# Performance work log

Hardware: AMD Instinct MI355X
Metric: run time of the kernel (lower is better)

Reference implementation:

```python
import jax, jax.numpy as jnp
import numpy as np

IN_FEATURES = 512
OUT_FEATURES = 256
BATCH = 1024


def setup_inputs() -> dict:
    key = jax.random.key(0)
    k1, k2, k3, k4 = jax.random.split(key, 4)
    n_lower = IN_FEATURES * (IN_FEATURES - 1) // 2  # strictly-lower triangle count
    return {
        "inputs": jax.random.normal(k1, (BATCH, IN_FEATURES), dtype=jnp.float32),
        "weight": jax.random.normal(k2, (OUT_FEATURES, 1, IN_FEATURES), dtype=jnp.float32),
        "L_diags": jax.random.uniform(k3, (OUT_FEATURES, IN_FEATURES), dtype=jnp.float32),
        "L_lower": jax.random.normal(k4, (OUT_FEATURES, n_lower), dtype=jnp.float32) * 0.05,
    }


def _build_L(L_diags, L_lower):
    # Per-class lower-triangular matrix: diag = L_diags**2, strict lower = L_lower.
    K, d = L_diags.shape
    ri, ci = np.tril_indices(d, k=-1)  # static index pattern (row-major, matches torch.tril_indices)
    diag_idx = jnp.arange(d)
    L = jnp.zeros((K, d, d), dtype=L_diags.dtype)
    L = L.at[:, diag_idx, diag_idx].set(jnp.square(L_diags))
    L = L.at[:, ri, ci].set(L_lower)
    return L  # [K, d, d]


def reference(inputs, weight, L_diags, L_lower):
    L = _build_L(L_diags, L_lower)                      # [K, d, d]
    pinputs = jnp.einsum('bd,kde->kbe', inputs, L)      # [K, B, d]
    pweights = jnp.einsum('kod,kde->koe', weight, L)    # [K, 1, d]
    dist = pinputs - pweights                           # broadcast over B -> [K, B, d]
    out = jnp.sqrt(jnp.sum(jnp.square(dist), axis=2))   # torch.norm(dim=2) -> [K, B]
    return out.T                                        # [B, K]
```

## Files before the change

kernel.cpp:

```cpp
#include <hip/hip_runtime.h>
#include <hip/hip_bf16.h>
#include <math.h>

#define B_SZ   1024
#define D_SZ   512
#define KC_SZ  256
#define NLOW   130816

#define STEP_ELEMS  8192
#define NSTEPS      20
#define CLASS_ELEMS (NSTEPS * STEP_ELEMS)

#define OFF_XP     (size_t)(KC_SZ * CLASS_ELEMS * 2)
#define OFF_TPART  (OFF_XP + 64 * STEP_ELEMS * 2)
#define OFF_T      (OFF_TPART + (size_t)KC_SZ * 8 * 512 * 4)
#define WS_NEED    (OFF_T + (size_t)KC_SZ * 512 * 4)

typedef __attribute__((ext_vector_type(4))) float  f32x4;
typedef __attribute__((ext_vector_type(4), aligned(4))) float f32x4u;
typedef __attribute__((ext_vector_type(8))) __bf16 bf16x8;

__device__ __forceinline__ int sbase_of(int ct) { return ct * (9 - ct); }
__device__ __forceinline__ int kch_of(int s) {
    return (s < 8) ? s : (s < 14) ? s - 6 : (s < 18) ? s - 10 : s - 12;
}

__global__ __launch_bounds__(256)
void prep_x(const float* __restrict__ X, __hip_bfloat16* __restrict__ Xp) {
    const int bx  = blockIdx.x;
    const int pg  = bx >> 2;
    const int mt  = pg >> 3, kch = pg & 7;
    __bf16* out = (__bf16*)Xp + (size_t)pg * STEP_ELEMS;
    const int line = threadIdx.x + (bx & 3) * 256;
    const int wmg = line >> 9, mi = (line >> 7) & 3, h = (line >> 6) & 1;
    const int lane = line & 63, q = lane >> 4, c = lane & 15;
    const int row = mt * 128 + wmg * 64 + mi * 16 + c;
    const float* src = X + (size_t)row * D_SZ + kch * 64 + h * 32 + q * 8;
    f32x4 v0 = ((const f32x4*)src)[0];
    f32x4 v1 = ((const f32x4*)src)[1];
    bf16x8 p;
    #pragma unroll
    for (int j = 0; j < 4; ++j) { p[j] = (__bf16)v0[j]; p[j + 4] = (__bf16)v1[j]; }
    *(bf16x8*)(out + line * 8) = p;
}

__global__ __launch_bounds__(256)
void prep_b(const float* __restrict__ Ldiag,
            const float* __restrict__ Llow,
            const float* __restrict__ W,
            __hip_bfloat16* __restrict__ Bp,
            float* __restrict__ tpart) {
    __shared__ __bf16 Lt[128 * 64];
    __shared__ float  ptl[32 * 129];

    const int s  = blockIdx.x;
    const int kc = blockIdx.y;
    const int ct = (s < 8) ? 0 : (s < 14) ? 1 : (s < 18) ? 2 : 3;
    const int dt = kch_of(s);
    const int e0 = ct << 7, d0 = dt << 6;

    const int tid = threadIdx.x;
    const int m   = tid & 31;
    const int seg = tid >> 5;
    const int es  = seg << 4;
    const int dg0 = d0 + 2 * m;

    int cls;
    if (dt >= 2 * ct + 2)      cls = 0;
    else if (dt == 2 * ct + 1) cls = (seg < 4) ? 0 : 1;
    else                       cls = (seg < 4) ? 1 : 2;

    const float* lowb = Llow + (size_t)kc * NLOW;
    const float2 wv = *(const float2*)(W + (size_t)kc * D_SZ + dg0);

    float v0[16], v1[16];
    if (cls == 0) {
        const int t0 = (dg0 * (dg0 - 1)) >> 1;
        const int t1 = t0 + dg0;
        const float* s0 = lowb + t0 + e0 + es;
        const float* s1 = lowb + t1 + e0 + es;
        #pragma unroll
        for (int i = 0; i < 4; ++i) {
            f32x4u a = ((const f32x4u*)s0)[i];
            f32x4u b = ((const f32x4u*)s1)[i];
            #pragma unroll
            for (int j = 0; j < 4; ++j) { v0[i * 4 + j] = a[j]; v1[i * 4 + j] = b[j]; }
        }
    } else if (cls == 1) {
        const int t0 = (dg0 * (dg0 - 1)) >> 1;
        const int t1 = t0 + dg0;
        const float* diagb = Ldiag + (size_t)kc * D_SZ;
        float q0 = diagb[dg0],     q1 = diagb[dg0 + 1];
        q0 *= q0; q1 *= q1;
        #pragma unroll
        for (int j = 0; j < 16; ++j) {
            const int eg = e0 + es + j;
            v0[j] = (eg < dg0)     ? lowb[t0 + eg] : ((eg == dg0)     ? q0 : 0.f);
            v1[j] = (eg < dg0 + 1) ? lowb[t1 + eg] : ((eg == dg0 + 1) ? q1 : 0.f);
        }
    } else {
        #pragma unroll
        for (int j = 0; j < 16; ++j) { v0[j] = 0.f; v1[j] = 0.f; }
    }

    char* ltb = (char*)Lt;
    #pragma unroll
    for (int j = 0; j < 16; ++j) {
        const int el = es + j;
        union { __bf16 h[2]; unsigned u; } pk;
        pk.h[0] = (__bf16)v0[j];
        pk.h[1] = (__bf16)v1[j];
        const int off = el * 128 + ((4 * m) ^ ((el & 7) << 4));
        *(unsigned*)(ltb + off) = pk.u;
        ptl[m * 129 + el] = wv.x * v0[j] + wv.y * v1[j];
    }
    __syncthreads();

    __bf16* page = (__bf16*)Bp + (size_t)kc * CLASS_ELEMS + (size_t)s * STEP_ELEMS;
    const int lane = tid & 63, q = lane >> 4, c = lane & 15;
    #pragma unroll
    for (int k = 0; k < 4; ++k) {
        const int ln = k * 256 + tid;
        const int up = ln >> 6;
        const int h  = up & 1;
        const int el = ((up >> 3) << 6) + (((up >> 1) & 3) << 4) + c;
        const int off = el * 128 + (((h << 6) + (q << 4)) ^ ((el & 7) << 4));
        *(bf16x8*)(page + (size_t)ln * 8) = *(const bf16x8*)(ltb + off);
    }

    if (tid < 128) {
        float sum = 0.f;
        #pragma unroll
        for (int mm = 0; mm < 32; ++mm) sum += ptl[mm * 129 + tid];
        tpart[((size_t)(kc * 8 + dt)) * 512 + e0 + tid] = sum;
    }
}

__global__ __launch_bounds__(256)
void t_reduce(const float* __restrict__ tpart, float* __restrict__ Tv) {
    const int idx = blockIdx.x * 256 + threadIdx.x;
    const int kc = idx >> 9, e = idx & 511;
    const int ct = e >> 7;
    float s = 0.f;
    for (int dt = ct << 1; dt < 8; ++dt)
        s += tpart[((size_t)(kc * 8 + dt)) * 512 + e];
    Tv[idx] = s;
}

__global__ __launch_bounds__(256, 2)
void gml2_main(const __hip_bfloat16* __restrict__ Xp,
               const __hip_bfloat16* __restrict__ Bp,
               const float* __restrict__ Tv,
               float* __restrict__ Out) {
    __shared__ __align__(16) char ldsbuf[2][32768];

    const int tid = threadIdx.x;
    const int bx  = blockIdx.x;
    const int xcd = bx & 7;
    const int g   = bx >> 3;
    const int kc  = xcd * 32 + (g >> 3);
    const int mt  = g & 7;

    const int lane = tid & 63;
    const int wave = tid >> 6;
    const int wmg  = wave & 1;
    const int wng  = wave >> 1;
    const int c    = lane & 15;
    const int q    = lane >> 4;

    const __bf16* pA = (const __bf16*)Xp + (size_t)(mt * 8) * STEP_ELEMS;
    const __bf16* pB = (const __bf16*)Bp + (size_t)kc * CLASS_ELEMS;

    float tvr[4][4];
    #pragma unroll
    for (int ct4 = 0; ct4 < 4; ++ct4)
        #pragma unroll
        for (int ni = 0; ni < 4; ++ni)
            tvr[ct4][ni] = Tv[kc * 512 + ct4 * 128 + wng * 64 + ni * 16 + c];

    int aoff[4][2], boff[4][2];
    #pragma unroll
    for (int mi = 0; mi < 4; ++mi)
        #pragma unroll
        for (int h = 0; h < 2; ++h)
            aoff[mi][h] = (((wmg * 4 + mi) * 2 + h) * 64 + lane) * 16;
    #pragma unroll
    for (int ni = 0; ni < 4; ++ni)
        #pragma unroll
        for (int h = 0; h < 2; ++h)
            boff[ni][h] = (((wng * 4 + ni) * 2 + h) * 64 + lane) * 16;

    f32x4 acc[4][4];
    #pragma unroll
    for (int mi = 0; mi < 4; ++mi)
        #pragma unroll
        for (int ni = 0; ni < 4; ++ni)
            acc[mi][ni] = (f32x4){0.f, 0.f, 0.f, 0.f};
    float rsum[16];
    #pragma unroll
    for (int i = 0; i < 16; ++i) rsum[i] = 0.f;

    bf16x8 fa[4][2], fb[4][2];

#define STAGE(BUF, SIDX) {                                                     \
    const int kch_ = kch_of(SIDX);                                             \
    const char* ga_ = (const char*)(pA + (size_t)kch_ * STEP_ELEMS);           \
    const char* gb_ = (const char*)(pB + (size_t)(SIDX) * STEP_ELEMS);         \
    char* la_ = &ldsbuf[BUF][0];                                               \
    char* lb_ = &ldsbuf[BUF][16384];                                           \
    _Pragma("unroll") for (int i_ = 0; i_ < 4; ++i_) {                         \
        const int ch_ = (wave * 4 + i_) * 1024;                                \
        __builtin_amdgcn_global_load_lds(                                      \
            (const __attribute__((address_space(1))) void*)(ga_ + ch_ + lane * 16), \
            (__attribute__((address_space(3))) void*)(la_ + ch_), 16, 0, 0);   \
        __builtin_amdgcn_global_load_lds(                                      \
            (const __attribute__((address_space(1))) void*)(gb_ + ch_ + lane * 16), \
            (__attribute__((address_space(3))) void*)(lb_ + ch_), 16, 0, 0);   \
    } }

#define LDS_FRAGS(BUF) {                                                       \
    const char* la_ = &ldsbuf[BUF][0];                                         \
    const char* lb_ = &ldsbuf[BUF][16384];                                     \
    _Pragma("unroll") for (int mi = 0; mi < 4; ++mi)                           \
    _Pragma("unroll") for (int h = 0; h < 2; ++h)                              \
        fa[mi][h] = *(const bf16x8*)(la_ + aoff[mi][h]);                       \
    _Pragma("unroll") for (int ni = 0; ni < 4; ++ni)                           \
    _Pragma("unroll") for (int h = 0; h < 2; ++h)                              \
        fb[ni][h] = *(const bf16x8*)(lb_ + boff[ni][h]); }

#define MFMA_ALL                                                               \
    _Pragma("unroll") for (int mi = 0; mi < 4; ++mi)                           \
    _Pragma("unroll") for (int ni = 0; ni < 4; ++ni)                           \
    _Pragma("unroll") for (int h = 0; h < 2; ++h)                              \
        acc[mi][ni] = __builtin_amdgcn_mfma_f32_16x16x32_bf16(                 \
            fa[mi][h], fb[ni][h], acc[mi][ni], 0, 0, 0);

#define FOLD(CT) {                                                             \
    _Pragma("unroll") for (int mi = 0; mi < 4; ++mi)                           \
    _Pragma("unroll") for (int ni = 0; ni < 4; ++ni)                           \
    _Pragma("unroll") for (int r = 0; r < 4; ++r) {                            \
        float y_ = acc[mi][ni][r] - tvr[CT][ni];                               \
        rsum[mi * 4 + r] += y_ * y_;                                           \
        acc[mi][ni][r] = 0.f; } }

    STAGE(0, 0);

    #pragma unroll
    for (int s = 0; s < NSTEPS; ++s) {
        const int cur = s & 1;
        if (s == 8)       { FOLD(0); }
        else if (s == 14) { FOLD(1); }
        else if (s == 18) { FOLD(2); }

        if (s + 1 < NSTEPS) {
            STAGE(cur ^ 1, s + 1);
            asm volatile("s_waitcnt vmcnt(8)" ::: "memory");
        } else {
            asm volatile("s_waitcnt vmcnt(0)" ::: "memory");
        }
        __builtin_amdgcn_s_barrier();

        LDS_FRAGS(cur);
        MFMA_ALL;

        __builtin_amdgcn_s_barrier();
    }
    FOLD(3);

    #pragma unroll
    for (int i = 0; i < 16; ++i) {
        float v = rsum[i];
        v += __shfl_xor(v, 1, 64);
        v += __shfl_xor(v, 2, 64);
        v += __shfl_xor(v, 4, 64);
        v += __shfl_xor(v, 8, 64);
        rsum[i] = v;
    }
    float (*osum)[128] = (float(*)[128])&ldsbuf[0][0];
    if (c == 0) {
        #pragma unroll
        for (int mi = 0; mi < 4; ++mi)
            #pragma unroll
            for (int r = 0; r < 4; ++r)
                osum[wng][wmg * 64 + mi * 16 + q * 4 + r] = rsum[mi * 4 + r];
    }
    __syncthreads();
    if (tid < 128) {
        float v = osum[0][tid] + osum[1][tid];
        Out[(size_t)(mt * 128 + tid) * KC_SZ + kc] = sqrtf(v);
    }
}

#define FLDA 40
#define BM 128
#define BN 128
__device__ __forceinline__ void fstep_map(int s, int& ct, int& k0) {
    if (s < 16)      { ct = 0; k0 = s * 32; }
    else if (s < 28) { ct = 1; k0 = 128 + (s - 16) * 32; }
    else if (s < 36) { ct = 2; k0 = 256 + (s - 28) * 32; }
    else             { ct = 3; k0 = 384 + (s - 36) * 32; }
}
__global__ __launch_bounds__(256, 2)
void gml2_fallback(const float* __restrict__ X, const float* __restrict__ W,
                   const float* __restrict__ Ldiag, const float* __restrict__ Llow,
                   float* __restrict__ Out) {
    __shared__ __bf16 As[BM * FLDA];
    __shared__ __bf16 Bs[BN * FLDA];
    __shared__ float  Ws[D_SZ];
    __shared__ float  osum[2][BM];
    const int tid = threadIdx.x;
    const int bx  = blockIdx.x;
    const int xcd = bx & 7;
    const int g   = bx >> 3;
    const int kc  = xcd * 32 + (g >> 3);
    const int mt  = g & 7;
    const int lane = tid & 63, wave = tid >> 6;
    const int wm = (wave & 1) * 64, wn = (wave >> 1) * 64;
    const int c = lane & 15, q = lane >> 4;
    const int am = tid >> 1, akh = (tid & 1) << 4;
    const float* xrow = X + (size_t)(mt * BM + am) * D_SZ;
    const float* wrow = W + (size_t)kc * D_SZ;
    const int be = tid & 127, bd = (tid >> 7) << 4;
    const float* lowbase  = Llow  + (size_t)kc * NLOW;
    const float* diagbase = Ldiag + (size_t)kc * D_SZ;
    if (tid < 128) ((f32x4*)Ws)[tid] = ((const f32x4*)wrow)[tid];
    float rsum[16];
    #pragma unroll
    for (int i = 0; i < 16; ++i) rsum[i] = 0.f;
    f32x4 acc[4][4];
    #pragma unroll
    for (int mi = 0; mi < 4; ++mi)
        #pragma unroll
        for (int ni = 0; ni < 4; ++ni) acc[mi][ni] = (f32x4){0.f, 0.f, 0.f, 0.f};
    f32x4 xr[4];
    float bb[16];
    auto prefetch = [&](int s) {
        int pct, pk0; fstep_map(s, pct, pk0);
        const int pe0 = pct * BN;
        const float* xp = xrow + pk0 + akh;
        #pragma unroll
        for (int i = 0; i < 4; ++i) xr[i] = ((const f32x4*)xp)[i];
        const int e = pe0 + be, d0 = pk0 + bd;
        int tri = (d0 * (d0 - 1)) >> 1;
        if (pk0 >= pe0 + BN) {
            #pragma unroll
            for (int j = 0; j < 16; ++j) { bb[j] = lowbase[tri + e]; tri += d0 + j; }
        } else {
            #pragma unroll
            for (int j = 0; j < 16; ++j) {
                const int d = d0 + j;
                float val = 0.f;
                if (d > e)       val = lowbase[tri + e];
                else if (d == e) { float dq = diagbase[d]; val = dq * dq; }
                bb[j] = val; tri += d;
            }
        }
    };
    prefetch(0);
    __syncthreads();
    int cur_ct = 0;
    for (int s = 0; s < 40; ++s) {
        int ct, k0; fstep_map(s, ct, k0);
        if (ct != cur_ct) {
            #pragma unroll
            for (int mi = 0; mi < 4; ++mi)
                #pragma unroll
                for (int ni = 0; ni < 4; ++ni)
                    #pragma unroll
                    for (int r = 0; r < 4; ++r) {
                        float y = acc[mi][ni][r];
                        rsum[mi * 4 + r] += y * y;
                        acc[mi][ni][r] = 0.f;
                    }
            cur_ct = ct;
        }
        bf16x8 ap0, ap1;
        {
            const f32x4* wsp = (const f32x4*)&Ws[k0 + akh];
            #pragma unroll
            for (int i = 0; i < 4; ++i) {
                f32x4 wv = wsp[i];
                #pragma unroll
                for (int l = 0; l < 4; ++l) {
                    float v = xr[i][l] - wv[l];
                    int idx = i * 4 + l;
                    if (idx < 8) ap0[idx] = (__bf16)v;
                    else         ap1[idx - 8] = (__bf16)v;
                }
            }
        }
        bf16x8 bp0, bp1;
        #pragma unroll
        for (int j = 0; j < 8; ++j) { bp0[j] = (__bf16)bb[j]; bp1[j] = (__bf16)bb[j + 8]; }
        __syncthreads();
        *(bf16x8*)&As[am * FLDA + akh]     = ap0;
        *(bf16x8*)&As[am * FLDA + akh + 8] = ap1;
        *(bf16x8*)&Bs[be * FLDA + bd]      = bp0;
        *(bf16x8*)&Bs[be * FLDA + bd + 8]  = bp1;
        if (s + 1 < 40) prefetch(s + 1);
        __syncthreads();
        bf16x8 af[4], bfr[4];
        #pragma unroll
        for (int mi = 0; mi < 4; ++mi)
            af[mi] = *(const bf16x8*)&As[(wm + mi * 16 + c) * FLDA + q * 8];
        #pragma unroll
        for (int ni = 0; ni < 4; ++ni)
            bfr[ni] = *(const bf16x8*)&Bs[(wn + ni * 16 + c) * FLDA + q * 8];
        #pragma unroll
        for (int mi = 0; mi < 4; ++mi)
            #pragma unroll
            for (int ni = 0; ni < 4; ++ni)
                acc[mi][ni] = __builtin_amdgcn_mfma_f32_16x16x32_bf16(
                    af[mi], bfr[ni], acc[mi][ni], 0, 0, 0);
    }
    #pragma unroll
    for (int mi = 0; mi < 4; ++mi)
        #pragma unroll
        for (int ni = 0; ni < 4; ++ni)
            #pragma unroll
            for (int r = 0; r < 4; ++r) {
                float y = acc[mi][ni][r];
                rsum[mi * 4 + r] += y * y;
            }
    #pragma unroll
    for (int i = 0; i < 16; ++i) {
        float s = rsum[i];
        s += __shfl_xor(s, 1, 64);
        s += __shfl_xor(s, 2, 64);
        s += __shfl_xor(s, 4, 64);
        s += __shfl_xor(s, 8, 64);
        rsum[i] = s;
    }
    const int wnIdx = wave >> 1;
    if (c == 0) {
        #pragma unroll
        for (int mi = 0; mi < 4; ++mi)
            #pragma unroll
            for (int r = 0; r < 4; ++r)
                osum[wnIdx][wm + mi * 16 + q * 4 + r] = rsum[mi * 4 + r];
    }
    __syncthreads();
    if (tid < BM) {
        float s = osum[0][tid] + osum[1][tid];
        Out[(size_t)(mt * BM + tid) * KC_SZ + kc] = sqrtf(s);
    }
}

extern "C" void kernel_launch(void* const* d_in, const int* in_sizes, int n_in,
                              void* d_out, int out_size, void* d_ws, size_t ws_size,
                              hipStream_t stream) {
    const float* X  = (const float*)d_in[0];
    const float* W  = (const float*)d_in[1];
    const float* Ld = (const float*)d_in[2];
    const float* Ll = (const float*)d_in[3];
    float* Out = (float*)d_out;

    if (ws_size >= WS_NEED) {
        __hip_bfloat16* Bp    = (__hip_bfloat16*)d_ws;
        __hip_bfloat16* Xp    = (__hip_bfloat16*)((char*)d_ws + OFF_XP);
        float*          tpart = (float*)((char*)d_ws + OFF_TPART);
        float*          Tvv   = (float*)((char*)d_ws + OFF_T);
        prep_x  <<<dim3(256),           dim3(256), 0, stream>>>(X, Xp);
        prep_b  <<<dim3(NSTEPS, KC_SZ), dim3(256), 0, stream>>>(Ld, Ll, W, Bp, tpart);
        t_reduce<<<dim3(512),           dim3(256), 0, stream>>>(tpart, Tvv);
        gml2_main<<<dim3(KC_SZ * 8),    dim3(256), 0, stream>>>(Xp, Bp, Tvv, Out);
    } else {
        gml2_fallback<<<dim3(KC_SZ * 8), dim3(256), 0, stream>>>(X, W, Ld, Ll, Out);
    }
}
```

Measured before the change: 302.7 us.

## Keep A-operand fragments resident in registers, stage only B through LDS

Loads all eight K-chunks of the input tile's MFMA fragments directly from global memory into registers once, before the main loop. Only the per-class B operand is now double-buffered through LDS. This halves per-step LDS staging and fragment reads, and shrinks shared memory to the B buffers plus a separate reduction array. In exchange, 256 extra VGPRs of fragment state are held per thread, which risks spilling or reduced occupancy under the two-blocks-per-CU launch bound.

```diff
diff --git a/kernel.cpp b/kernel.cpp
--- a/kernel.cpp
+++ b/kernel.cpp
@@ -152,7 +152,8 @@
                const __hip_bfloat16* __restrict__ Bp,
                const float* __restrict__ Tv,
                float* __restrict__ Out) {
-    __shared__ __align__(16) char ldsbuf[2][32768];
+    __shared__ __align__(16) char bbuf[2][16384];
+    __shared__ float osum[2][128];
 
     const int tid = threadIdx.x;
     const int bx  = blockIdx.x;
@@ -178,17 +179,15 @@
         for (int ni = 0; ni < 4; ++ni)
             tvr[ct4][ni] = Tv[kc * 512 + ct4 * 128 + wng * 64 + ni * 16 + c];
 
-    int aoff[4][2], boff[4][2];
-    #pragma unroll
-    for (int mi = 0; mi < 4; ++mi)
-        #pragma unroll
-        for (int h = 0; h < 2; ++h)
-            aoff[mi][h] = (((wmg * 4 + mi) * 2 + h) * 64 + lane) * 16;
-    #pragma unroll
-    for (int ni = 0; ni < 4; ++ni)
-        #pragma unroll
-        for (int h = 0; h < 2; ++h)
-            boff[ni][h] = (((wng * 4 + ni) * 2 + h) * 64 + lane) * 16;
+    bf16x8 fa[8][4][2];
+    #pragma unroll
+    for (int kch = 0; kch < 8; ++kch)
+        #pragma unroll
+        for (int mi = 0; mi < 4; ++mi)
+            #pragma unroll
+            for (int h = 0; h < 2; ++h)
+                fa[kch][mi][h] = *(const bf16x8*)(pA + (size_t)kch * STEP_ELEMS
+                                  + ((((wmg * 4 + mi) * 2 + h) * 64) + lane) * 8);
 
     f32x4 acc[4][4];
     #pragma unroll
@@ -200,40 +199,15 @@
     #pragma unroll
     for (int i = 0; i < 16; ++i) rsum[i] = 0.f;
 
-    bf16x8 fa[4][2], fb[4][2];
-
-#define STAGE(BUF, SIDX) {                                                     \
-    const int kch_ = kch_of(SIDX);                                             \
-    const char* ga_ = (const char*)(pA + (size_t)kch_ * STEP_ELEMS);           \
-    const char* gb_ = (const char*)(pB + (size_t)(SIDX) * STEP_ELEMS);         \
-    char* la_ = &ldsbuf[BUF][0];                                               \
-    char* lb_ = &ldsbuf[BUF][16384];                                           \
+#define STAGE_B(BUF, SP) {                                                     \
+    const char* gb_ = (const char*)(pB + (size_t)(SP) * STEP_ELEMS);           \
+    char* lb_ = &bbuf[BUF][0];                                                 \
     _Pragma("unroll") for (int i_ = 0; i_ < 4; ++i_) {                         \
         const int ch_ = (wave * 4 + i_) * 1024;                                \
-        __builtin_amdgcn_global_load_lds(                                      \
-            (const __attribute__((address_space(1))) void*)(ga_ + ch_ + lane * 16), \
-            (__attribute__((address_space(3))) void*)(la_ + ch_), 16, 0, 0);   \
         __builtin_amdgcn_global_load_lds(                                      \
             (const __attribute__((address_space(1))) void*)(gb_ + ch_ + lane * 16), \
             (__attribute__((address_space(3))) void*)(lb_ + ch_), 16, 0, 0);   \
     } }
-
-#define LDS_FRAGS(BUF) {                                                       \
-    const char* la_ = &ldsbuf[BUF][0];                                         \
-    const char* lb_ = &ldsbuf[BUF][16384];                                     \
-    _Pragma("unroll") for (int mi = 0; mi < 4; ++mi)                           \
-    _Pragma("unroll") for (int h = 0; h < 2; ++h)                              \
-        fa[mi][h] = *(const bf16x8*)(la_ + aoff[mi][h]);                       \
-    _Pragma("unroll") for (int ni = 0; ni < 4; ++ni)                           \
-    _Pragma("unroll") for (int h = 0; h < 2; ++h)                              \
-        fb[ni][h] = *(const bf16x8*)(lb_ + boff[ni][h]); }
-
-#define MFMA_ALL                                                               \
-    _Pragma("unroll") for (int mi = 0; mi < 4; ++mi)                           \
-    _Pragma("unroll") for (int ni = 0; ni < 4; ++ni)                           \
-    _Pragma("unroll") for (int h = 0; h < 2; ++h)                              \
-        acc[mi][ni] = __builtin_amdgcn_mfma_f32_16x16x32_bf16(                 \
-            fa[mi][h], fb[ni][h], acc[mi][ni], 0, 0, 0);
 
 #define FOLD(CT) {                                                             \
     _Pragma("unroll") for (int mi = 0; mi < 4; ++mi)                           \
@@ -243,25 +217,40 @@
         rsum[mi * 4 + r] += y_ * y_;                                           \
         acc[mi][ni][r] = 0.f; } }
 
-    STAGE(0, 0);
+    STAGE_B(0, 0);
 
     #pragma unroll
     for (int s = 0; s < NSTEPS; ++s) {
         const int cur = s & 1;
+        const int kch = kch_of(s);
         if (s == 8)       { FOLD(0); }
         else if (s == 14) { FOLD(1); }
         else if (s == 18) { FOLD(2); }
 
         if (s + 1 < NSTEPS) {
-            STAGE(cur ^ 1, s + 1);
-            asm volatile("s_waitcnt vmcnt(8)" ::: "memory");
+            STAGE_B(cur ^ 1, s + 1);
+            asm volatile("s_waitcnt vmcnt(4)" ::: "memory");
         } else {
             asm volatile("s_waitcnt vmcnt(0)" ::: "memory");
         }
         __builtin_amdgcn_s_barrier();
 
-        LDS_FRAGS(cur);
-        MFMA_ALL;
+        bf16x8 fb[4][2];
+        #pragma unroll
+        for (int ni = 0; ni < 4; ++ni)
+            #pragma unroll
+            for (int h = 0; h < 2; ++h)
+                fb[ni][h] = *(const bf16x8*)(&bbuf[cur][0]
+                              + ((((wng * 4 + ni) * 2 + h) * 64) + lane) * 16);
+
+        #pragma unroll
+        for (int h = 0; h < 2; ++h)
+            #pragma unroll
+            for (int mi = 0; mi < 4; ++mi)
+                #pragma unroll
+                for (int ni = 0; ni < 4; ++ni)
+                    acc[mi][ni] = __builtin_amdgcn_mfma_f32_16x16x32_bf16(
+                        fa[kch][mi][h], fb[ni][h], acc[mi][ni], 0, 0, 0);
 
         __builtin_amdgcn_s_barrier();
     }
@@ -276,7 +265,6 @@
         v += __shfl_xor(v, 8, 64);
         rsum[i] = v;
     }
-    float (*osum)[128] = (float(*)[128])&ldsbuf[0][0];
     if (c == 0) {
         #pragma unroll
         for (int mi = 0; mi < 4; ++mi)
```

Result: slower. 602.9 us (+99.2%).

## Merge prep kernels, fold T reduction into main, skip zero upper-triangle pages

Applied to the files above, without the earlier changes.

Merges prep_x and prep_b into one launch and removes the t_reduce kernel. The main kernel now reduces the T partial sums into shared memory itself. On diagonal tiles where half of the B page is zero (upper triangle), the change stages only half of B and lets only one wave-column group do the MFMAs. The goal is to cut launch overhead and redundant loads and matrix work on the triangular diagonal blocks. In exchange it adds per-block reduction work and load imbalance across waves, and it relies on the per-step vmcnt counts being correct.

```diff
diff --git a/kernel.cpp b/kernel.cpp
--- a/kernel.cpp
+++ b/kernel.cpp
@@ -26,40 +26,48 @@
 }
 
 __global__ __launch_bounds__(256)
-void prep_x(const float* __restrict__ X, __hip_bfloat16* __restrict__ Xp) {
-    const int bx  = blockIdx.x;
-    const int pg  = bx >> 2;
-    const int mt  = pg >> 3, kch = pg & 7;
-    __bf16* out = (__bf16*)Xp + (size_t)pg * STEP_ELEMS;
-    const int line = threadIdx.x + (bx & 3) * 256;
-    const int wmg = line >> 9, mi = (line >> 7) & 3, h = (line >> 6) & 1;
-    const int lane = line & 63, q = lane >> 4, c = lane & 15;
-    const int row = mt * 128 + wmg * 64 + mi * 16 + c;
-    const float* src = X + (size_t)row * D_SZ + kch * 64 + h * 32 + q * 8;
-    f32x4 v0 = ((const f32x4*)src)[0];
-    f32x4 v1 = ((const f32x4*)src)[1];
-    bf16x8 p;
-    #pragma unroll
-    for (int j = 0; j < 4; ++j) { p[j] = (__bf16)v0[j]; p[j + 4] = (__bf16)v1[j]; }
-    *(bf16x8*)(out + line * 8) = p;
-}
-
-__global__ __launch_bounds__(256)
-void prep_b(const float* __restrict__ Ldiag,
-            const float* __restrict__ Llow,
-            const float* __restrict__ W,
-            __hip_bfloat16* __restrict__ Bp,
-            float* __restrict__ tpart) {
+void prep_all(const float* __restrict__ X,
+              const float* __restrict__ Ldiag,
+              const float* __restrict__ Llow,
+              const float* __restrict__ W,
+              __hip_bfloat16* __restrict__ Xp,
+              __hip_bfloat16* __restrict__ Bp,
+              float* __restrict__ tpart) {
     __shared__ __bf16 Lt[128 * 64];
     __shared__ float  ptl[32 * 129];
 
-    const int s  = blockIdx.x;
-    const int kc = blockIdx.y;
+    const int bx  = blockIdx.x;
+    const int tid = threadIdx.x;
+
+    if (bx < 64) {
+        const int pg  = bx;
+        const int mt  = pg >> 3, kch = pg & 7;
+        __bf16* out = (__bf16*)Xp + (size_t)pg * STEP_ELEMS;
+        #pragma unroll
+        for (int i = 0; i < 4; ++i) {
+            const int line = tid + i * 256;
+            const int wmg = line >> 9, mi = (line >> 7) & 3, h = (line >> 6) & 1;
+            const int lane = line & 63, q = lane >> 4, c = lane & 15;
+            const int row = mt * 128 + wmg * 64 + mi * 16 + c;
+            const float* src = X + (size_t)row * D_SZ + kch * 64 + h * 32 + q * 8;
+            f32x4 v0 = ((const f32x4*)src)[0];
+            f32x4 v1 = ((const f32x4*)src)[1];
+            bf16x8 p;
+            #pragma unroll
+            for (int j = 0; j < 4; ++j) { p[j] = (__bf16)v0[j]; p[j + 4] = (__bf16)v1[j]; }
+            *(bf16x8*)(out + line * 8) = p;
+        }
+        return;
+    }
+
+    const int idx = bx - 64;
+    const int s   = idx % 20;
+    const int kc  = idx / 20;
     const int ct = (s < 8) ? 0 : (s < 14) ? 1 : (s < 18) ? 2 : 3;
     const int dt = kch_of(s);
     const int e0 = ct << 7, d0 = dt << 6;
-
-    const int tid = threadIdx.x;
+    const bool zpage = (dt == 2 * ct);
+
     const int m   = tid & 31;
     const int seg = tid >> 5;
     const int es  = seg << 4;
@@ -120,6 +128,7 @@
     const int lane = tid & 63, q = lane >> 4, c = lane & 15;
     #pragma unroll
     for (int k = 0; k < 4; ++k) {
+        if (zpage && k >= 2) continue;
         const int ln = k * 256 + tid;
         const int up = ln >> 6;
         const int h  = up & 1;
@@ -136,23 +145,13 @@
     }
 }
 
-__global__ __launch_bounds__(256)
-void t_reduce(const float* __restrict__ tpart, float* __restrict__ Tv) {
-    const int idx = blockIdx.x * 256 + threadIdx.x;
-    const int kc = idx >> 9, e = idx & 511;
-    const int ct = e >> 7;
-    float s = 0.f;
-    for (int dt = ct << 1; dt < 8; ++dt)
-        s += tpart[((size_t)(kc * 8 + dt)) * 512 + e];
-    Tv[idx] = s;
-}
-
 __global__ __launch_bounds__(256, 2)
 void gml2_main(const __hip_bfloat16* __restrict__ Xp,
                const __hip_bfloat16* __restrict__ Bp,
-               const float* __restrict__ Tv,
+               const float* __restrict__ tpart,
                float* __restrict__ Out) {
     __shared__ __align__(16) char ldsbuf[2][32768];
+    __shared__ float tvs[512];
 
     const int tid = threadIdx.x;
     const int bx  = blockIdx.x;
@@ -171,13 +170,6 @@
     const __bf16* pA = (const __bf16*)Xp + (size_t)(mt * 8) * STEP_ELEMS;
     const __bf16* pB = (const __bf16*)Bp + (size_t)kc * CLASS_ELEMS;
 
-    float tvr[4][4];
-    #pragma unroll
-    for (int ct4 = 0; ct4 < 4; ++ct4)
-        #pragma unroll
-        for (int ni = 0; ni < 4; ++ni)
-            tvr[ct4][ni] = Tv[kc * 512 + ct4 * 128 + wng * 64 + ni * 16 + c];
-
     int aoff[4][2], boff[4][2];
     #pragma unroll
     for (int mi = 0; mi < 4; ++mi)
@@ -200,9 +192,7 @@
     #pragma unroll
     for (int i = 0; i < 16; ++i) rsum[i] = 0.f;
 
-    bf16x8 fa[4][2], fb[4][2];
-
-#define STAGE(BUF, SIDX) {                                                     \
+#define STAGE(BUF, SIDX, NB) {                                                 \
     const int kch_ = kch_of(SIDX);                                             \
     const char* ga_ = (const char*)(pA + (size_t)kch_ * STEP_ELEMS);           \
     const char* gb_ = (const char*)(pB + (size_t)(SIDX) * STEP_ELEMS);         \
@@ -213,59 +203,74 @@
         __builtin_amdgcn_global_load_lds(                                      \
             (const __attribute__((address_space(1))) void*)(ga_ + ch_ + lane * 16), \
             (__attribute__((address_space(3))) void*)(la_ + ch_), 16, 0, 0);   \
+    }                                                                          \
+    _Pragma("unroll") for (int i_ = 0; i_ < (NB); ++i_) {                      \
+        const int ch_ = (wave * (NB) + i_) * 1024;                             \
         __builtin_amdgcn_global_load_lds(                                      \
             (const __attribute__((address_space(1))) void*)(gb_ + ch_ + lane * 16), \
             (__attribute__((address_space(3))) void*)(lb_ + ch_), 16, 0, 0);   \
     } }
 
-#define LDS_FRAGS(BUF) {                                                       \
-    const char* la_ = &ldsbuf[BUF][0];                                         \
-    const char* lb_ = &ldsbuf[BUF][16384];                                     \
-    _Pragma("unroll") for (int mi = 0; mi < 4; ++mi)                           \
-    _Pragma("unroll") for (int h = 0; h < 2; ++h)                              \
-        fa[mi][h] = *(const bf16x8*)(la_ + aoff[mi][h]);                       \
+#define WAIT8 asm volatile("s_waitcnt vmcnt(8)" ::: "memory")
+#define WAIT6 asm volatile("s_waitcnt vmcnt(6)" ::: "memory")
+#define WAIT0 asm volatile("s_waitcnt vmcnt(0)" ::: "memory")
+
+#define GSTEP(S, ZS, NBN, WMAC) {                                              \
+    if ((S) + 1 < NSTEPS) STAGE(((S) + 1) & 1, (S) + 1, NBN);                  \
+    WMAC;                                                                      \
+    __builtin_amdgcn_s_barrier();                                              \
+    if (!(ZS) || wng == 0) {                                                   \
+        const char* la_ = &ldsbuf[(S) & 1][0];                                 \
+        const char* lb_ = &ldsbuf[(S) & 1][16384];                             \
+        bf16x8 fa[4][2], fb[4][2];                                             \
+        _Pragma("unroll") for (int mi = 0; mi < 4; ++mi)                       \
+        _Pragma("unroll") for (int h = 0; h < 2; ++h)                          \
+            fa[mi][h] = *(const bf16x8*)(la_ + aoff[mi][h]);                   \
+        _Pragma("unroll") for (int ni = 0; ni < 4; ++ni)                       \
+        _Pragma("unroll") for (int h = 0; h < 2; ++h)                          \
+            fb[ni][h] = *(const bf16x8*)(lb_ + boff[ni][h]);                   \
+        _Pragma("unroll") for (int h = 0; h < 2; ++h)                          \
+        _Pragma("unroll") for (int mi = 0; mi < 4; ++mi)                       \
+        _Pragma("unroll") for (int ni = 0; ni < 4; ++ni)                       \
+            acc[mi][ni] = __builtin_amdgcn_mfma_f32_16x16x32_bf16(             \
+                fa[mi][h], fb[ni][h], acc[mi][ni], 0, 0, 0);                   \
+    }                                                                          \
+    __builtin_amdgcn_s_barrier(); }
+
+#define FOLD(CT) {                                                             \
+    float tv_[4];                                                              \
     _Pragma("unroll") for (int ni = 0; ni < 4; ++ni)                           \
-    _Pragma("unroll") for (int h = 0; h < 2; ++h)                              \
-        fb[ni][h] = *(const bf16x8*)(lb_ + boff[ni][h]); }
-
-#define MFMA_ALL                                                               \
-    _Pragma("unroll") for (int mi = 0; mi < 4; ++mi)                           \
-    _Pragma("unroll") for (int ni = 0; ni < 4; ++ni)                           \
-    _Pragma("unroll") for (int h = 0; h < 2; ++h)                              \
-        acc[mi][ni] = __builtin_amdgcn_mfma_f32_16x16x32_bf16(                 \
-            fa[mi][h], fb[ni][h], acc[mi][ni], 0, 0, 0);
-
-#define FOLD(CT) {                                                             \
+        tv_[ni] = tvs[(CT) * 128 + wng * 64 + ni * 16 + c];                    \
     _Pragma("unroll") for (int mi = 0; mi < 4; ++mi)                           \
     _Pragma("unroll") for (int ni = 0; ni < 4; ++ni)                           \
     _Pragma("unroll") for (int r = 0; r < 4; ++r) {                            \
-        float y_ = acc[mi][ni][r] - tvr[CT][ni];                               \
+        float y_ = acc[mi][ni][r] - tv_[ni];                                   \
         rsum[mi * 4 + r] += y_ * y_;                                           \
         acc[mi][ni][r] = 0.f; } }
 
-    STAGE(0, 0);
-
-    #pragma unroll
-    for (int s = 0; s < NSTEPS; ++s) {
-        const int cur = s & 1;
-        if (s == 8)       { FOLD(0); }
-        else if (s == 14) { FOLD(1); }
-        else if (s == 18) { FOLD(2); }
-
-        if (s + 1 < NSTEPS) {
-            STAGE(cur ^ 1, s + 1);
-            asm volatile("s_waitcnt vmcnt(8)" ::: "memory");
-        } else {
-            asm volatile("s_waitcnt vmcnt(0)" ::: "memory");
-        }
-        __builtin_amdgcn_s_barrier();
-
-        LDS_FRAGS(cur);
-        MFMA_ALL;
-
-        __builtin_amdgcn_s_barrier();
-    }
-    FOLD(3);
+    STAGE(0, 0, 2);
+
+    if (tid < 128) {
+        const int ctq = tid >> 5;
+        f32x4 ssum = (f32x4){0.f, 0.f, 0.f, 0.f};
+        for (int dt = ctq << 1; dt < 8; ++dt)
+            ssum += ((const f32x4*)(tpart + ((size_t)(kc * 8 + dt)) * 512))[tid];
+        ((f32x4*)tvs)[tid] = ssum;
+    }
+    __syncthreads();
+
+    GSTEP(0, 1, 4, WAIT8) GSTEP(1, 0, 4, WAIT8) GSTEP(2, 0, 4, WAIT8)
+    GSTEP(3, 0, 4, WAIT8) GSTEP(4, 0, 4, WAIT8) GSTEP(5, 0, 4, WAIT8)
+    GSTEP(6, 0, 4, WAIT8) GSTEP(7, 0, 2, WAIT6)
+    FOLD(0)
+    GSTEP(8, 1, 4, WAIT8) GSTEP(9, 0, 4, WAIT8) GSTEP(10, 0, 4, WAIT8)
+    GSTEP(11, 0, 4, WAIT8) GSTEP(12, 0, 4, WAIT8) GSTEP(13, 0, 2, WAIT6)
+    FOLD(1)
+    GSTEP(14, 1, 4, WAIT8) GSTEP(15, 0, 4, WAIT8) GSTEP(16, 0, 4, WAIT8)
+    GSTEP(17, 0, 2, WAIT6)
+    FOLD(2)
+    GSTEP(18, 1, 4, WAIT8) GSTEP(19, 0, 4, WAIT0)
+    FOLD(3)
 
     #pragma unroll
     for (int i = 0; i < 16; ++i) {
@@ -459,11 +464,9 @@
         __hip_bfloat16* Bp    = (__hip_bfloat16*)d_ws;
         __hip_bfloat16* Xp    = (__hip_bfloat16*)((char*)d_ws + OFF_XP);
         float*          tpart = (float*)((char*)d_ws + OFF_TPART);
-        float*          Tvv   = (float*)((char*)d_ws + OFF_T);
-        prep_x  <<<dim3(256),           dim3(256), 0, stream>>>(X, Xp);
-        prep_b  <<<dim3(NSTEPS, KC_SZ), dim3(256), 0, stream>>>(Ld, Ll, W, Bp, tpart);
-        t_reduce<<<dim3(512),           dim3(256), 0, stream>>>(tpart, Tvv);
-        gml2_main<<<dim3(KC_SZ * 8),    dim3(256), 0, stream>>>(Xp, Bp, Tvv, Out);
+        prep_all<<<dim3(64 + NSTEPS * KC_SZ), dim3(256), 0, stream>>>(
+            X, Ld, Ll, W, Xp, Bp, tpart);
+        gml2_main<<<dim3(KC_SZ * 8), dim3(256), 0, stream>>>(Xp, Bp, tpart, Out);
     } else {
         gml2_fallback<<<dim3(KC_SZ * 8), dim3(256), 0, stream>>>(X, W, Ld, Ll, Out);
     }
```

Result: slower. 347.0 us (+14.7%).

## Merge prep kernels and fold T reduction into main kernel

Applied to the files above, without the earlier changes.

Combines the X conversion and B packing kernels into one launch, with the first 64 blocks doing the X packing, each now handling four lines per thread. Removes the separate t_reduce kernel: each main-kernel block sums the partial T values for its class into shared memory after issuing its first stage load. This drops two kernel launches and their inter-kernel gaps. In exchange, every one of the 8 row-tile blocks per class redoes the same small reduction, and a block-wide barrier is added before the main loop.

```diff
diff --git a/kernel.cpp b/kernel.cpp
--- a/kernel.cpp
+++ b/kernel.cpp
@@ -13,8 +13,7 @@
 
 #define OFF_XP     (size_t)(KC_SZ * CLASS_ELEMS * 2)
 #define OFF_TPART  (OFF_XP + 64 * STEP_ELEMS * 2)
-#define OFF_T      (OFF_TPART + (size_t)KC_SZ * 8 * 512 * 4)
-#define WS_NEED    (OFF_T + (size_t)KC_SZ * 512 * 4)
+#define WS_NEED    (OFF_TPART + (size_t)KC_SZ * 8 * 512 * 4)
 
 typedef __attribute__((ext_vector_type(4))) float  f32x4;
 typedef __attribute__((ext_vector_type(4), aligned(4))) float f32x4u;
@@ -26,40 +25,47 @@
 }
 
 __global__ __launch_bounds__(256)
-void prep_x(const float* __restrict__ X, __hip_bfloat16* __restrict__ Xp) {
-    const int bx  = blockIdx.x;
-    const int pg  = bx >> 2;
-    const int mt  = pg >> 3, kch = pg & 7;
-    __bf16* out = (__bf16*)Xp + (size_t)pg * STEP_ELEMS;
-    const int line = threadIdx.x + (bx & 3) * 256;
-    const int wmg = line >> 9, mi = (line >> 7) & 3, h = (line >> 6) & 1;
-    const int lane = line & 63, q = lane >> 4, c = lane & 15;
-    const int row = mt * 128 + wmg * 64 + mi * 16 + c;
-    const float* src = X + (size_t)row * D_SZ + kch * 64 + h * 32 + q * 8;
-    f32x4 v0 = ((const f32x4*)src)[0];
-    f32x4 v1 = ((const f32x4*)src)[1];
-    bf16x8 p;
-    #pragma unroll
-    for (int j = 0; j < 4; ++j) { p[j] = (__bf16)v0[j]; p[j + 4] = (__bf16)v1[j]; }
-    *(bf16x8*)(out + line * 8) = p;
-}
-
-__global__ __launch_bounds__(256)
-void prep_b(const float* __restrict__ Ldiag,
-            const float* __restrict__ Llow,
-            const float* __restrict__ W,
-            __hip_bfloat16* __restrict__ Bp,
-            float* __restrict__ tpart) {
+void prep_all(const float* __restrict__ X,
+              const float* __restrict__ Ldiag,
+              const float* __restrict__ Llow,
+              const float* __restrict__ W,
+              __hip_bfloat16* __restrict__ Xp,
+              __hip_bfloat16* __restrict__ Bp,
+              float* __restrict__ tpart) {
     __shared__ __bf16 Lt[128 * 64];
     __shared__ float  ptl[32 * 129];
 
-    const int s  = blockIdx.x;
-    const int kc = blockIdx.y;
+    const int bx  = blockIdx.x;
+    const int tid = threadIdx.x;
+
+    if (bx < 64) {
+        const int pg  = bx;
+        const int mt  = pg >> 3, kch = pg & 7;
+        __bf16* out = (__bf16*)Xp + (size_t)pg * STEP_ELEMS;
+        #pragma unroll
+        for (int i = 0; i < 4; ++i) {
+            const int line = tid + i * 256;
+            const int wmg = line >> 9, mi = (line >> 7) & 3, h = (line >> 6) & 1;
+            const int lane = line & 63, q = lane >> 4, c = lane & 15;
+            const int row = mt * 128 + wmg * 64 + mi * 16 + c;
+            const float* src = X + (size_t)row * D_SZ + kch * 64 + h * 32 + q * 8;
+            f32x4 v0 = ((const f32x4*)src)[0];
+            f32x4 v1 = ((const f32x4*)src)[1];
+            bf16x8 p;
+            #pragma unroll
+            for (int j = 0; j < 4; ++j) { p[j] = (__bf16)v0[j]; p[j + 4] = (__bf16)v1[j]; }
+            *(bf16x8*)(out + line * 8) = p;
+        }
+        return;
+    }
+
+    const int idx = bx - 64;
+    const int s   = idx % 20;
+    const int kc  = idx / 20;
     const int ct = (s < 8) ? 0 : (s < 14) ? 1 : (s < 18) ? 2 : 3;
     const int dt = kch_of(s);
     const int e0 = ct << 7, d0 = dt << 6;
 
-    const int tid = threadIdx.x;
     const int m   = tid & 31;
     const int seg = tid >> 5;
     const int es  = seg << 4;
@@ -136,23 +142,13 @@
     }
 }
 
-__global__ __launch_bounds__(256)
-void t_reduce(const float* __restrict__ tpart, float* __restrict__ Tv) {
-    const int idx = blockIdx.x * 256 + threadIdx.x;
-    const int kc = idx >> 9, e = idx & 511;
-    const int ct = e >> 7;
-    float s = 0.f;
-    for (int dt = ct << 1; dt < 8; ++dt)
-        s += tpart[((size_t)(kc * 8 + dt)) * 512 + e];
-    Tv[idx] = s;
-}
-
 __global__ __launch_bounds__(256, 2)
 void gml2_main(const __hip_bfloat16* __restrict__ Xp,
                const __hip_bfloat16* __restrict__ Bp,
-               const float* __restrict__ Tv,
+               const float* __restrict__ tpart,
                float* __restrict__ Out) {
     __shared__ __align__(16) char ldsbuf[2][32768];
+    __shared__ float tvs[512];
 
     const int tid = threadIdx.x;
     const int bx  = blockIdx.x;
@@ -170,13 +166,6 @@
 
     const __bf16* pA = (const __bf16*)Xp + (size_t)(mt * 8) * STEP_ELEMS;
     const __bf16* pB = (const __bf16*)Bp + (size_t)kc * CLASS_ELEMS;
-
-    float tvr[4][4];
-    #pragma unroll
-    for (int ct4 = 0; ct4 < 4; ++ct4)
-        #pragma unroll
-        for (int ni = 0; ni < 4; ++ni)
-            tvr[ct4][ni] = Tv[kc * 512 + ct4 * 128 + wng * 64 + ni * 16 + c];
 
     int aoff[4][2], boff[4][2];
     #pragma unroll
@@ -244,6 +233,22 @@
         acc[mi][ni][r] = 0.f; } }
 
     STAGE(0, 0);
+
+    if (tid < 128) {
+        const int ctq = tid >> 5;
+        f32x4 ssum = (f32x4){0.f, 0.f, 0.f, 0.f};
+        for (int dt = ctq << 1; dt < 8; ++dt)
+            ssum += ((const f32x4*)(tpart + ((size_t)(kc * 8 + dt)) * 512))[tid];
+        ((f32x4*)tvs)[tid] = ssum;
+    }
+    __syncthreads();
+
+    float tvr[4][4];
+    #pragma unroll
+    for (int ct4 = 0; ct4 < 4; ++ct4)
+        #pragma unroll
+        for (int ni = 0; ni < 4; ++ni)
+            tvr[ct4][ni] = tvs[ct4 * 128 + wng * 64 + ni * 16 + c];
 
     #pragma unroll
     for (int s = 0; s < NSTEPS; ++s) {
@@ -459,11 +464,9 @@
         __hip_bfloat16* Bp    = (__hip_bfloat16*)d_ws;
         __hip_bfloat16* Xp    = (__hip_bfloat16*)((char*)d_ws + OFF_XP);
         float*          tpart = (float*)((char*)d_ws + OFF_TPART);
-        float*          Tvv   = (float*)((char*)d_ws + OFF_T);
-        prep_x  <<<dim3(256),           dim3(256), 0, stream>>>(X, Xp);
-        prep_b  <<<dim3(NSTEPS, KC_SZ), dim3(256), 0, stream>>>(Ld, Ll, W, Bp, tpart);
-        t_reduce<<<dim3(512),           dim3(256), 0, stream>>>(tpart, Tvv);
-        gml2_main<<<dim3(KC_SZ * 8),    dim3(256), 0, stream>>>(Xp, Bp, Tvv, Out);
+        prep_all<<<dim3(64 + NSTEPS * KC_SZ), dim3(256), 0, stream>>>(
+            X, Ld, Ll, W, Xp, Bp, tpart);
+        gml2_main<<<dim3(KC_SZ * 8), dim3(256), 0, stream>>>(Xp, Bp, tpart, Out);
     } else {
         gml2_fallback<<<dim3(KC_SZ * 8), dim3(256), 0, stream>>>(X, W, Ld, Ll, Out);
     }
```

Result: no change. 307.2 us (+1.5%).
